# Kernel optimization log

Measured on AMD Instinct MI355X. Metric: run time of the kernel, lower is better.

## Reference

```python
import jax, jax.numpy as jnp
import numpy as np

N = 50000
E = 800000
H, C = 8, 16          # heads, per-head channels (H*C = 128)
G = 64                # number of graphs
EPS = 1e-5


def setup_inputs() -> dict:
    key = jax.random.key(0)
    ks = jax.random.split(key, 8)
    x = jax.random.normal(ks[0], (N, 128), dtype=jnp.float32)
    edge_index = jax.random.randint(ks[1], (2, E), 0, N, dtype=jnp.int64)
    batch = jnp.sort(jax.random.randint(ks[2], (N,), 0, G, dtype=jnp.int64))
    W = jax.random.normal(ks[3], (3, 128, 128), dtype=jnp.float32) * 0.08
    att_src = jax.random.normal(ks[4], (3, H, C), dtype=jnp.float32) * 0.1
    att_dst = jax.random.normal(ks[5], (3, H, C), dtype=jnp.float32) * 0.1
    bias = jnp.zeros((3, 128), dtype=jnp.float32)
    gamma = jnp.ones((3, 128), dtype=jnp.float32)
    beta = jnp.zeros((3, 128), dtype=jnp.float32)
    ro_w = jax.random.normal(ks[6], (128, 2), dtype=jnp.float32) * 0.08
    ro_b = jnp.zeros((2,), dtype=jnp.float32)
    return {"x": x, "edge_index": edge_index, "batch": batch, "W": W,
            "att_src": att_src, "att_dst": att_dst, "bias": bias,
            "gamma": gamma, "beta": beta, "ro_w": ro_w, "ro_b": ro_b}


def _gat_block(prev, h, src, dst, W, a_s, a_d, b, g, be):
    # GATConv (concat=True, add_self_loops already applied to src/dst)
    xp = (h @ W).reshape(N, H, C)                       # [N,H,C]
    al_s = jnp.sum(xp * a_s, axis=-1)                   # [N,H]
    al_d = jnp.sum(xp * a_d, axis=-1)                   # [N,H]
    logits = jax.nn.leaky_relu(al_s[src] + al_d[dst], negative_slope=0.2)  # [Et,H]
    m = jax.ops.segment_max(logits, dst, num_segments=N)        # softmax over dst groups
    ex = jnp.exp(logits - m[dst])
    denom = jax.ops.segment_sum(ex, dst, num_segments=N)
    alpha = ex / denom[dst]                              # [Et,H]
    msg = xp[src] * alpha[:, :, None]                    # [Et,H,C]
    agg = jax.ops.segment_sum(msg, dst, num_segments=N).reshape(N, H * C) + b
    y = prev + agg
    # BatchNorm1d (training mode: batch stats, biased variance)
    mu = y.mean(axis=0)
    var = y.var(axis=0)
    yn = (y - mu) / jnp.sqrt(var + EPS) * g + be
    return jax.nn.elu(yn)


def reference(x, edge_index, batch, W, att_src, att_dst, bias, gamma, beta, ro_w, ro_b):
    loops = jnp.arange(N, dtype=edge_index.dtype)
    src = jnp.concatenate([edge_index[0], loops])        # PyG add_self_loops=True
    dst = jnp.concatenate([edge_index[1], loops])
    h = x
    prev = jnp.zeros((N, 128), dtype=x.dtype)
    for i in range(3):
        out = _gat_block(prev, h, src, dst, W[i], att_src[i], att_dst[i],
                         bias[i], gamma[i], beta[i])
        prev = h[:, :128]
        h = out
    # global mean pool over graphs
    sums = jax.ops.segment_sum(h, batch, num_segments=G)
    cnt = jax.ops.segment_sum(jnp.ones((N,), dtype=h.dtype), batch, num_segments=G)
    pooled = sums / jnp.maximum(cnt, 1.0)[:, None]
    return pooled @ ro_w + ro_b
```

## Files before the change

### kernel.cpp

```cpp
#include <hip/hip_runtime.h>
#include <hip/hip_bf16.h>
#include <math.h>

#define NN 50000
#define EE 800000
#define MM (EE + NN)
#define GG 64
#define SWG 512
#define NSB ((NN + 255) / 256)
#define PSP 16

__device__ __forceinline__ int geti(const void* p, long idx, int is64) {
    return is64 ? (int)((const long long*)p)[idx] : ((const int*)p)[idx];
}

__device__ __forceinline__ float bf2f(unsigned short u) {
    return __uint_as_float(((unsigned)u) << 16);
}

__global__ void k_detect(const int* __restrict__ ei, int* __restrict__ flag) {
    if (blockIdx.x == 0 && threadIdx.x == 0) {
        int ok = 1;
        for (int k = 0; k < 128; ++k) {
            int lo = ei[2 * k], hi = ei[2 * k + 1];
            if (hi != 0 || (unsigned)lo >= (unsigned)NN) { ok = 0; break; }
        }
        flag[0] = ok;
    }
}


__global__ void k_zero(int* p, int n) {
    int i = blockIdx.x * blockDim.x + threadIdx.x;
    if (i < n) p[i] = 0;
}

__global__ void k_count(const void* __restrict__ ei, const int* __restrict__ flag,
                        int* __restrict__ counts) {
    int e = blockIdx.x * blockDim.x + threadIdx.x;
    if (e >= MM) return;
    int is64 = flag[0];
    int d = (e < EE) ? geti(ei, (long)EE + e, is64) : (e - EE);
    if ((unsigned)d < (unsigned)NN) atomicAdd(&counts[d], 1);
}

__global__ __launch_bounds__(256) void k_scan1(const int* __restrict__ counts,
                                               int* __restrict__ rowptr,
                                               int* __restrict__ bsum) {
    __shared__ int buf[256];
    int b = blockIdx.x, tid = threadIdx.x;
    int i = b * 256 + tid;
    int v = (i < NN) ? counts[i] : 0;
    buf[tid] = v;
    __syncthreads();
    for (int off = 1; off < 256; off <<= 1) {
        int t = (tid >= off) ? buf[tid - off] : 0;
        __syncthreads();
        buf[tid] += t;
        __syncthreads();
    }
    if (i < NN) rowptr[i + 1] = buf[tid];
    if (tid == 255) bsum[b] = buf[255];
}

__global__ __launch_bounds__(256) void k_scan2(int* __restrict__ bsum) {
    __shared__ int buf[256];
    int tid = threadIdx.x;
    int v = (tid < NSB) ? bsum[tid] : 0;
    buf[tid] = v;
    __syncthreads();
    for (int off = 1; off < 256; off <<= 1) {
        int t = (tid >= off) ? buf[tid - off] : 0;
        __syncthreads();
        buf[tid] += t;
        __syncthreads();
    }
    if (tid < NSB) bsum[tid] = (tid == 0) ? 0 : buf[tid - 1];
}

__global__ __launch_bounds__(256) void k_scan3(int* __restrict__ rowptr,
                                               const int* __restrict__ bsum) {
    int b = blockIdx.x, tid = threadIdx.x;
    int i = b * 256 + tid;
    if (i < NN) rowptr[i + 1] += bsum[b];
    if (b == 0 && tid == 0) rowptr[0] = 0;
}

__global__ void k_fill(const void* __restrict__ ei, const int* __restrict__ flag,
                       const int* __restrict__ rowptr,
                       int* __restrict__ fill, int* __restrict__ colv) {
    int e = blockIdx.x * blockDim.x + threadIdx.x;
    if (e >= MM) return;
    int is64 = flag[0];
    int s, d;
    if (e < EE) { s = geti(ei, e, is64); d = geti(ei, (long)EE + e, is64); }
    else { s = d = e - EE; }
    if ((unsigned)d >= (unsigned)NN || (unsigned)s >= (unsigned)NN) return;
    int pos = rowptr[d] + atomicAdd(&fill[d], 1);
    if ((unsigned)pos < (unsigned)MM) colv[pos] = s;
}


__global__ __launch_bounds__(256) void k_gemm_att(
    const float* __restrict__ h, const float* __restrict__ W,
    const float* __restrict__ attS, const float* __restrict__ attD,
    unsigned short* __restrict__ xpb, float* __restrict__ als,
    float* __restrict__ ald, int n)
{
    __shared__ float Wt[32][128];
    __shared__ float Ht[128][33];
    int tid = threadIdx.x;
    int head = tid & 7, r0 = tid >> 3;
    int rbase = blockIdx.x * 128;

    float acc[4][16];
#pragma unroll
    for (int a = 0; a < 4; ++a)
#pragma unroll
        for (int b = 0; b < 16; ++b) acc[a][b] = 0.f;

    for (int k0 = 0; k0 < 128; k0 += 32) {
#pragma unroll
        for (int j = 0; j < 4; ++j) {
            int idx = tid * 16 + j * 4;
            int kk = idx >> 7, c = idx & 127;
            *(float4*)&Wt[kk][c] = *(const float4*)&W[(k0 + kk) * 128 + c];
        }
#pragma unroll
        for (int j = 0; j < 4; ++j) {
            int f = tid * 16 + j * 4;
            int r = f >> 5, kk = f & 31;
            int gr = rbase + r;
            float4 v = make_float4(0.f, 0.f, 0.f, 0.f);
            if (gr < n) v = *(const float4*)&h[gr * 128 + k0 + kk];
            Ht[r][kk] = v.x; Ht[r][kk + 1] = v.y; Ht[r][kk + 2] = v.z; Ht[r][kk + 3] = v.w;
        }
        __syncthreads();
#pragma unroll
        for (int kk = 0; kk < 32; ++kk) {
            float wv[16];
#pragma unroll
            for (int j = 0; j < 4; ++j)
                *(float4*)&wv[j * 4] = *(const float4*)&Wt[kk][head * 16 + j * 4];
#pragma unroll
            for (int rr = 0; rr < 4; ++rr) {
                float hv = Ht[r0 + rr * 32][kk];
#pragma unroll
                for (int j = 0; j < 16; ++j) acc[rr][j] = fmaf(hv, wv[j], acc[rr][j]);
            }
        }
        __syncthreads();
    }

    float asv[16], adv[16];
#pragma unroll
    for (int j = 0; j < 16; ++j) { asv[j] = attS[head * 16 + j]; adv[j] = attD[head * 16 + j]; }

#pragma unroll
    for (int rr = 0; rr < 4; ++rr) {
        int r = rbase + r0 + rr * 32;
        if (r < n) {
            float ds = 0.f, dd = 0.f;
#pragma unroll
            for (int j = 0; j < 16; ++j) { ds = fmaf(acc[rr][j], asv[j], ds); dd = fmaf(acc[rr][j], adv[j], dd); }
            als[r * 8 + head] = ds;
            ald[r * 8 + head] = dd;
            unsigned short xb[16];
#pragma unroll
            for (int j = 0; j < 16; ++j) {
                __hip_bfloat16 t = __float2bfloat16(acc[rr][j]);
                xb[j] = *reinterpret_cast<unsigned short*>(&t);
            }
            *(uint4*)&xpb[r * 128 + head * 16]     = *(uint4*)&xb[0];
            *(uint4*)&xpb[r * 128 + head * 16 + 8] = *(uint4*)&xb[8];
        }
    }
}


__global__ __launch_bounds__(256) void k_agg(
    const unsigned short* __restrict__ xpb, const float* __restrict__ als,
    const float* __restrict__ ald,
    const int* __restrict__ rowptr, const int* __restrict__ colv,
    const float* __restrict__ prev, const float* __restrict__ bias,
    float* __restrict__ y, int n)
{
    __shared__ float alds[4][8][8];
    __shared__ int   slds[4][8];
    int wv = threadIdx.x >> 6;
    int wid = (int)((blockIdx.x * blockDim.x + threadIdx.x) >> 6);
    int lane = threadIdx.x & 63;
    if (wid >= n) return;
    int rs = rowptr[wid], re = rowptr[wid + 1];
    int deg = re - rs;

    int hd = lane & 7;
    int ee = lane >> 3;
    float aldn = ald[wid * 8 + hd];

    float sm = 0.f;
    for (int b = ee; b < deg; b += 8) {
        int s = colv[rs + b];
        float v = als[s * 8 + hd] + aldn;
        v = v > 0.f ? v : 0.2f * v;
        sm += expf(v);
    }
    sm += __shfl_xor(sm, 8);
    sm += __shfl_xor(sm, 16);
    sm += __shfl_xor(sm, 32);

    float inv = 1.f / sm;
    int q = lane >> 3;
    int c0 = lane * 2;

    float a0 = 0.f, a1 = 0.f;
    int full = deg & ~7;

    for (int b0 = 0; b0 < full; b0 += 8) {
        int se = colv[rs + b0 + ee];
        float v = als[se * 8 + hd] + aldn;
        v = v > 0.f ? v : 0.2f * v;
        float al = expf(v) * inv;
        alds[wv][ee][hd] = al;
        if (hd == 0) slds[wv][ee] = se;
#pragma unroll
        for (int j = 0; j < 8; ++j) {
            int s = slds[wv][j];
            float a = alds[wv][j][q];
            ushort2 xv = *(const ushort2*)(xpb + (size_t)s * 128 + c0);
            a0 = fmaf(a, bf2f(xv.x), a0);
            a1 = fmaf(a, bf2f(xv.y), a1);
        }
    }

    if (full < deg) {
        int nb = deg - full;
        float al = 0.f;
        int se = 0;
        if (ee < nb) {
            se = colv[rs + full + ee];
            float v = als[se * 8 + hd] + aldn;
            v = v > 0.f ? v : 0.2f * v;
            al = expf(v) * inv;
        }
        alds[wv][ee][hd] = al;
        if (hd == 0) slds[wv][ee] = se;
        for (int j = 0; j < nb; ++j) {
            int s = slds[wv][j];
            float a = alds[wv][j][q];
            ushort2 xv = *(const ushort2*)(xpb + (size_t)s * 128 + c0);
            a0 = fmaf(a, bf2f(xv.x), a0);
            a1 = fmaf(a, bf2f(xv.y), a1);
        }
    }

    float p0 = prev ? prev[wid * 128 + c0] : 0.f;
    float p1 = prev ? prev[wid * 128 + c0 + 1] : 0.f;
    y[wid * 128 + c0] = p0 + a0 + bias[c0];
    y[wid * 128 + c0 + 1] = p1 + a1 + bias[c0 + 1];
}


__global__ __launch_bounds__(256) void k_stats(const float* __restrict__ y,
                                               double* __restrict__ partial, int n) {
    int col = threadIdx.x & 127;
    int rg = threadIdx.x >> 7;
    double s = 0.0, s2 = 0.0;
    for (int r = blockIdx.x * 2 + rg; r < n; r += SWG * 2) {
        float v = y[r * 128 + col];
        s += v; s2 += (double)v * (double)v;
    }
    __shared__ double ls[256], ls2[256];
    ls[threadIdx.x] = s; ls2[threadIdx.x] = s2;
    __syncthreads();
    if (rg == 0) {
        s += ls[threadIdx.x + 128];
        s2 += ls2[threadIdx.x + 128];
        partial[col * SWG + blockIdx.x] = s;
        partial[128 * SWG + col * SWG + blockIdx.x] = s2;
    }
}

__global__ void k_stats_fin(const double* __restrict__ partial, float* __restrict__ stats, int n) {
    int col = threadIdx.x;
    double s = 0.0, s2 = 0.0;
    for (int w = 0; w < SWG; ++w) {
        s += partial[col * SWG + w];
        s2 += partial[128 * SWG + col * SWG + w];
    }
    double mu = s / n;
    double var = s2 / n - mu * mu;
    stats[col] = (float)mu;
    stats[128 + col] = (float)(1.0 / sqrt(var + 1e-5));
}

__global__ __launch_bounds__(256) void k_elem(const float* __restrict__ y,
                                              const float* __restrict__ stats,
                                              const float* __restrict__ gamma,
                                              const float* __restrict__ beta,
                                              float* __restrict__ out, int total)
{
    int i = blockIdx.x * blockDim.x + threadIdx.x;
    if (i >= total) return;
    int col = i & 127;
    float v = (y[i] - stats[col]) * stats[128 + col] * gamma[col] + beta[col];
    out[i] = v > 0.f ? v : expm1f(v);
}


__global__ __launch_bounds__(256) void k_pool_part(
    const float* __restrict__ h, const void* __restrict__ batch,
    const int* __restrict__ flag, float* __restrict__ ppart, int n)
{
    int g = blockIdx.x / PSP;
    int sp = blockIdx.x % PSP;
    int is64 = flag[0];
    int lo = 0, hi = n;
    while (lo < hi) { int mid = (lo + hi) >> 1; if (geti(batch, mid, is64) < g) lo = mid + 1; else hi = mid; }
    int start = lo;
    hi = n;
    while (lo < hi) { int mid = (lo + hi) >> 1; if (geti(batch, mid, is64) < g + 1) lo = mid + 1; else hi = mid; }
    int end = lo;
    int cnt = end - start;
    int slice = (cnt + PSP - 1) / PSP;
    int s0 = start + sp * slice;
    int s1 = s0 + slice; if (s1 > end) s1 = end;

    int col = threadIdx.x & 127;
    int half = threadIdx.x >> 7;
    float s = 0.f;
    for (int r = s0 + half; r < s1; r += 2) s += h[r * 128 + col];
    __shared__ float ls[256];
    ls[threadIdx.x] = s;
    __syncthreads();
    if (half == 0) ppart[(g * PSP + sp) * 128 + col] = s + ls[col + 128];
}

__global__ __launch_bounds__(128) void k_pool_fin(
    const float* __restrict__ ppart, const void* __restrict__ batch,
    const int* __restrict__ flag, const float* __restrict__ row,
    const float* __restrict__ rob, float* __restrict__ out, int n)
{
    int g = blockIdx.x;
    int is64 = flag[0];
    int lo = 0, hi = n;
    while (lo < hi) { int mid = (lo + hi) >> 1; if (geti(batch, mid, is64) < g) lo = mid + 1; else hi = mid; }
    int start = lo;
    hi = n;
    while (lo < hi) { int mid = (lo + hi) >> 1; if (geti(batch, mid, is64) < g + 1) lo = mid + 1; else hi = mid; }
    int cnt = lo - start;

    int col = threadIdx.x;
    float s = 0.f;
#pragma unroll
    for (int sp = 0; sp < PSP; ++sp) s += ppart[(g * PSP + sp) * 128 + col];
    __shared__ float ls[128];
    ls[col] = s * (1.f / fmaxf((float)cnt, 1.f));
    __syncthreads();
    if (col < 2) {
        float acc = 0.f;
        for (int c = 0; c < 128; ++c) acc = fmaf(ls[c], row[c * 2 + col], acc);
        out[g * 2 + col] = acc + rob[col];
    }
}


extern "C" void kernel_launch(void* const* d_in, const int* in_sizes, int n_in,
                              void* d_out, int out_size, void* d_ws, size_t ws_size,
                              hipStream_t stream) {
    const float* x     = (const float*)d_in[0];
    const void*  ei    = d_in[1];
    const void*  batch = d_in[2];
    const float* W     = (const float*)d_in[3];
    const float* attS  = (const float*)d_in[4];
    const float* attD  = (const float*)d_in[5];
    const float* bias  = (const float*)d_in[6];
    const float* gamma = (const float*)d_in[7];
    const float* beta  = (const float*)d_in[8];
    const float* row   = (const float*)d_in[9];
    const float* rob   = (const float*)d_in[10];
    float* out = (float*)d_out;

    char* wsb = (char*)d_ws;
    size_t off = 0;
    auto alloc = [&](size_t bytes) {
        void* p = wsb + off;
        off += (bytes + 255) & ~(size_t)255;
        return p;
    };
    int*    flag    = (int*)alloc(256);
    int*    rowptr  = (int*)alloc((size_t)(NN + 1) * 4);
    int*    cnts    = (int*)alloc((size_t)NN * 4 * 2);
    int*    bsum    = (int*)alloc((size_t)256 * 4);
    int*    colv    = (int*)alloc((size_t)MM * 4);
    double* partial = (double*)alloc((size_t)128 * SWG * 2 * 8);
    float*  stats   = (float*)alloc(256 * 4);
    float*  ppart   = (float*)alloc((size_t)GG * PSP * 128 * 4);
    float*  ALS     = (float*)alloc((size_t)NN * 8 * 4);
    float*  ALD     = (float*)alloc((size_t)NN * 8 * 4);
    unsigned short* XPB = (unsigned short*)alloc((size_t)NN * 128 * 2);
    float* Y   = (float*)alloc((size_t)NN * 128 * 4);
    float* HB1 = (float*)alloc((size_t)NN * 128 * 4);
    float* HB2 = (float*)alloc((size_t)NN * 128 * 4);
    float* H3  = (float*)alloc((size_t)NN * 128 * 4);
    (void)ws_size; (void)in_sizes; (void)n_in; (void)out_size;

    int* fill = cnts + NN;
    const int GE = (NN * 128 + 255) / 256;

    hipLaunchKernelGGL(k_detect, dim3(1), dim3(64), 0, stream, (const int*)ei, flag);
    hipLaunchKernelGGL(k_zero, dim3((2 * NN + 255) / 256), dim3(256), 0, stream, cnts, 2 * NN);
    hipLaunchKernelGGL(k_count, dim3((MM + 255) / 256), dim3(256), 0, stream, ei, flag, cnts);
    hipLaunchKernelGGL(k_scan1, dim3(NSB), dim3(256), 0, stream, cnts, rowptr, bsum);
    hipLaunchKernelGGL(k_scan2, dim3(1), dim3(256), 0, stream, bsum);
    hipLaunchKernelGGL(k_scan3, dim3(NSB), dim3(256), 0, stream, rowptr, bsum);
    hipLaunchKernelGGL(k_fill, dim3((MM + 255) / 256), dim3(256), 0, stream, ei, flag, rowptr, fill, colv);

    const float* hs[4] = { x, HB1, HB2, H3 };
    for (int b = 0; b < 3; ++b) {
        const float* h = hs[b];
        const float* prev = (b == 0) ? nullptr : hs[b - 1];
        float* hn = (float*)hs[b + 1];

        hipLaunchKernelGGL(k_gemm_att, dim3((NN + 127) / 128), dim3(256), 0, stream,
                           h, W + b * 16384, attS + b * 128, attD + b * 128, XPB, ALS, ALD, NN);
        hipLaunchKernelGGL(k_agg, dim3((NN + 3) / 4), dim3(256), 0, stream,
                           XPB, ALS, ALD, rowptr, colv, prev, bias + b * 128, Y, NN);
        hipLaunchKernelGGL(k_stats, dim3(SWG), dim3(256), 0, stream, Y, partial, NN);
        hipLaunchKernelGGL(k_stats_fin, dim3(1), dim3(128), 0, stream, partial, stats, NN);
        hipLaunchKernelGGL(k_elem, dim3(GE), dim3(256), 0, stream,
                           Y, stats, gamma + b * 128, beta + b * 128, hn, NN * 128);
    }

    hipLaunchKernelGGL(k_pool_part, dim3(GG * PSP), dim3(256), 0, stream,
                       hs[3], batch, flag, ppart, NN);
    hipLaunchKernelGGL(k_pool_fin, dim3(GG), dim3(128), 0, stream,
                       ppart, batch, flag, row, rob, out, NN);
}
```

Measured before the change: 581.6 us.

## Fuse BatchNorm+ELU into consumer kernels and drop the elementwise pass

The separate BatchNorm-apply+ELU kernel is removed. The stats kernel now emits a folded per-column scale and shift, and the normalize+ELU is recomputed on the fly wherever the activation is consumed: the GEMM tile load, the residual 'prev' read in aggregation, and the final pooling. This saves a full N×128 read and write per layer plus three launches, at the cost of redundant expm1 evaluations and keeping three raw Y buffers alive.

```diff
diff --git a/kernel.cpp b/kernel.cpp
--- a/kernel.cpp
+++ b/kernel.cpp
@@ -16,6 +16,10 @@
 
 __device__ __forceinline__ float bf2f(unsigned short u) {
     return __uint_as_float(((unsigned)u) << 16);
+}
+
+__device__ __forceinline__ float eluf(float z) {
+    return z > 0.f ? z : expm1f(z);
 }
 
 __global__ void k_detect(const int* __restrict__ ei, int* __restrict__ flag) {
@@ -102,7 +106,8 @@
 
 
 __global__ __launch_bounds__(256) void k_gemm_att(
-    const float* __restrict__ h, const float* __restrict__ W,
+    const float* __restrict__ hsrc, const float* __restrict__ Ysrc,
+    const float* __restrict__ st, const float* __restrict__ W,
     const float* __restrict__ attS, const float* __restrict__ attD,
     unsigned short* __restrict__ xpb, float* __restrict__ als,
     float* __restrict__ ald, int n)
@@ -112,6 +117,7 @@
     int tid = threadIdx.x;
     int head = tid & 7, r0 = tid >> 3;
     int rbase = blockIdx.x * 128;
+    bool useY = (Ysrc != nullptr);
 
     float acc[4][16];
 #pragma unroll
@@ -132,7 +138,19 @@
             int r = f >> 5, kk = f & 31;
             int gr = rbase + r;
             float4 v = make_float4(0.f, 0.f, 0.f, 0.f);
-            if (gr < n) v = *(const float4*)&h[gr * 128 + k0 + kk];
+            if (gr < n) {
+                if (useY) {
+                    float4 yv = *(const float4*)&Ysrc[gr * 128 + k0 + kk];
+                    float4 scv = *(const float4*)&st[k0 + kk];
+                    float4 shv = *(const float4*)&st[128 + k0 + kk];
+                    v.x = eluf(fmaf(yv.x, scv.x, shv.x));
+                    v.y = eluf(fmaf(yv.y, scv.y, shv.y));
+                    v.z = eluf(fmaf(yv.z, scv.z, shv.z));
+                    v.w = eluf(fmaf(yv.w, scv.w, shv.w));
+                } else {
+                    v = *(const float4*)&hsrc[gr * 128 + k0 + kk];
+                }
+            }
             Ht[r][kk] = v.x; Ht[r][kk + 1] = v.y; Ht[r][kk + 2] = v.z; Ht[r][kk + 3] = v.w;
         }
         __syncthreads();
@@ -182,7 +200,8 @@
     const unsigned short* __restrict__ xpb, const float* __restrict__ als,
     const float* __restrict__ ald,
     const int* __restrict__ rowptr, const int* __restrict__ colv,
-    const float* __restrict__ prev, const float* __restrict__ bias,
+    const float* __restrict__ prevRaw, const float* __restrict__ prevY,
+    const float* __restrict__ pst, const float* __restrict__ bias,
     float* __restrict__ y, int n)
 {
     __shared__ float alds[4][8][8];
@@ -254,8 +273,15 @@
         }
     }
 
-    float p0 = prev ? prev[wid * 128 + c0] : 0.f;
-    float p1 = prev ? prev[wid * 128 + c0 + 1] : 0.f;
+    float p0 = 0.f, p1 = 0.f;
+    if (prevY) {
+        float2 yv = *(const float2*)(prevY + (size_t)wid * 128 + c0);
+        p0 = eluf(fmaf(yv.x, pst[c0], pst[128 + c0]));
+        p1 = eluf(fmaf(yv.y, pst[c0 + 1], pst[129 + c0]));
+    } else if (prevRaw) {
+        p0 = prevRaw[(size_t)wid * 128 + c0];
+        p1 = prevRaw[(size_t)wid * 128 + c0 + 1];
+    }
     y[wid * 128 + c0] = p0 + a0 + bias[c0];
     y[wid * 128 + c0 + 1] = p1 + a1 + bias[c0 + 1];
 }
@@ -281,7 +307,10 @@
     }
 }
 
-__global__ void k_stats_fin(const double* __restrict__ partial, float* __restrict__ stats, int n) {
+__global__ void k_stats_fin(const double* __restrict__ partial,
+                            const float* __restrict__ gamma,
+                            const float* __restrict__ beta,
+                            float* __restrict__ st, int n) {
     int col = threadIdx.x;
     double s = 0.0, s2 = 0.0;
     for (int w = 0; w < SWG; ++w) {
@@ -290,27 +319,17 @@
     }
     double mu = s / n;
     double var = s2 / n - mu * mu;
-    stats[col] = (float)mu;
-    stats[128 + col] = (float)(1.0 / sqrt(var + 1e-5));
-}
-
-__global__ __launch_bounds__(256) void k_elem(const float* __restrict__ y,
-                                              const float* __restrict__ stats,
-                                              const float* __restrict__ gamma,
-                                              const float* __restrict__ beta,
-                                              float* __restrict__ out, int total)
-{
-    int i = blockIdx.x * blockDim.x + threadIdx.x;
-    if (i >= total) return;
-    int col = i & 127;
-    float v = (y[i] - stats[col]) * stats[128 + col] * gamma[col] + beta[col];
-    out[i] = v > 0.f ? v : expm1f(v);
+    double rsig = 1.0 / sqrt(var + 1e-5);
+    double sc = (double)gamma[col] * rsig;
+    st[col] = (float)sc;
+    st[128 + col] = (float)((double)beta[col] - mu * sc);
 }
 
 
 __global__ __launch_bounds__(256) void k_pool_part(
-    const float* __restrict__ h, const void* __restrict__ batch,
-    const int* __restrict__ flag, float* __restrict__ ppart, int n)
+    const float* __restrict__ Y, const float* __restrict__ st,
+    const void* __restrict__ batch, const int* __restrict__ flag,
+    float* __restrict__ ppart, int n)
 {
     int g = blockIdx.x / PSP;
     int sp = blockIdx.x % PSP;
@@ -328,8 +347,10 @@
 
     int col = threadIdx.x & 127;
     int half = threadIdx.x >> 7;
+    float sc = st[col], sh = st[128 + col];
     float s = 0.f;
-    for (int r = s0 + half; r < s1; r += 2) s += h[r * 128 + col];
+    for (int r = s0 + half; r < s1; r += 2)
+        s += eluf(fmaf(Y[(size_t)r * 128 + col], sc, sh));
     __shared__ float ls[256];
     ls[threadIdx.x] = s;
     __syncthreads();
@@ -394,19 +415,21 @@
     int*    bsum    = (int*)alloc((size_t)256 * 4);
     int*    colv    = (int*)alloc((size_t)MM * 4);
     double* partial = (double*)alloc((size_t)128 * SWG * 2 * 8);
-    float*  stats   = (float*)alloc(256 * 4);
+    float*  st1     = (float*)alloc(256 * 4);
+    float*  st2     = (float*)alloc(256 * 4);
+    float*  st3     = (float*)alloc(256 * 4);
     float*  ppart   = (float*)alloc((size_t)GG * PSP * 128 * 4);
     float*  ALS     = (float*)alloc((size_t)NN * 8 * 4);
     float*  ALD     = (float*)alloc((size_t)NN * 8 * 4);
     unsigned short* XPB = (unsigned short*)alloc((size_t)NN * 128 * 2);
-    float* Y   = (float*)alloc((size_t)NN * 128 * 4);
-    float* HB1 = (float*)alloc((size_t)NN * 128 * 4);
-    float* HB2 = (float*)alloc((size_t)NN * 128 * 4);
-    float* H3  = (float*)alloc((size_t)NN * 128 * 4);
+    float* Y1 = (float*)alloc((size_t)NN * 128 * 4);
+    float* Y2 = (float*)alloc((size_t)NN * 128 * 4);
+    float* Y3 = (float*)alloc((size_t)NN * 128 * 4);
     (void)ws_size; (void)in_sizes; (void)n_in; (void)out_size;
 
     int* fill = cnts + NN;
-    const int GE = (NN * 128 + 255) / 256;
+    const int GB = (NN + 127) / 128;
+    const int GA = (NN + 3) / 4;
 
     hipLaunchKernelGGL(k_detect, dim3(1), dim3(64), 0, stream, (const int*)ei, flag);
     hipLaunchKernelGGL(k_zero, dim3((2 * NN + 255) / 256), dim3(256), 0, stream, cnts, 2 * NN);
@@ -416,24 +439,38 @@
     hipLaunchKernelGGL(k_scan3, dim3(NSB), dim3(256), 0, stream, rowptr, bsum);
     hipLaunchKernelGGL(k_fill, dim3((MM + 255) / 256), dim3(256), 0, stream, ei, flag, rowptr, fill, colv);
 
-    const float* hs[4] = { x, HB1, HB2, H3 };
-    for (int b = 0; b < 3; ++b) {
-        const float* h = hs[b];
-        const float* prev = (b == 0) ? nullptr : hs[b - 1];
-        float* hn = (float*)hs[b + 1];
-
-        hipLaunchKernelGGL(k_gemm_att, dim3((NN + 127) / 128), dim3(256), 0, stream,
-                           h, W + b * 16384, attS + b * 128, attD + b * 128, XPB, ALS, ALD, NN);
-        hipLaunchKernelGGL(k_agg, dim3((NN + 3) / 4), dim3(256), 0, stream,
-                           XPB, ALS, ALD, rowptr, colv, prev, bias + b * 128, Y, NN);
-        hipLaunchKernelGGL(k_stats, dim3(SWG), dim3(256), 0, stream, Y, partial, NN);
-        hipLaunchKernelGGL(k_stats_fin, dim3(1), dim3(128), 0, stream, partial, stats, NN);
-        hipLaunchKernelGGL(k_elem, dim3(GE), dim3(256), 0, stream,
-                           Y, stats, gamma + b * 128, beta + b * 128, hn, NN * 128);
-    }
+    hipLaunchKernelGGL(k_gemm_att, dim3(GB), dim3(256), 0, stream,
+                       x, (const float*)nullptr, (const float*)nullptr,
+                       W, attS, attD, XPB, ALS, ALD, NN);
+    hipLaunchKernelGGL(k_agg, dim3(GA), dim3(256), 0, stream,
+                       XPB, ALS, ALD, rowptr, colv,
+                       (const float*)nullptr, (const float*)nullptr, (const float*)nullptr,
+                       bias, Y1, NN);
+    hipLaunchKernelGGL(k_stats, dim3(SWG), dim3(256), 0, stream, Y1, partial, NN);
+    hipLaunchKernelGGL(k_stats_fin, dim3(1), dim3(128), 0, stream, partial, gamma, beta, st1, NN);
+
+    hipLaunchKernelGGL(k_gemm_att, dim3(GB), dim3(256), 0, stream,
+                       (const float*)nullptr, Y1, st1,
+                       W + 16384, attS + 128, attD + 128, XPB, ALS, ALD, NN);
+    hipLaunchKernelGGL(k_agg, dim3(GA), dim3(256), 0, stream,
+                       XPB, ALS, ALD, rowptr, colv,
+                       x, (const float*)nullptr, (const float*)nullptr,
+                       bias + 128, Y2, NN);
+    hipLaunchKernelGGL(k_stats, dim3(SWG), dim3(256), 0, stream, Y2, partial, NN);
+    hipLaunchKernelGGL(k_stats_fin, dim3(1), dim3(128), 0, stream, partial, gamma + 128, beta + 128, st2, NN);
+
+    hipLaunchKernelGGL(k_gemm_att, dim3(GB), dim3(256), 0, stream,
+                       (const float*)nullptr, Y2, st2,
+                       W + 32768, attS + 256, attD + 256, XPB, ALS, ALD, NN);
+    hipLaunchKernelGGL(k_agg, dim3(GA), dim3(256), 0, stream,
+                       XPB, ALS, ALD, rowptr, colv,
+                       (const float*)nullptr, Y1, st1,
+                       bias + 256, Y3, NN);
+    hipLaunchKernelGGL(k_stats, dim3(SWG), dim3(256), 0, stream, Y3, partial, NN);
+    hipLaunchKernelGGL(k_stats_fin, dim3(1), dim3(128), 0, stream, partial, gamma + 256, beta + 256, st3, NN);
 
     hipLaunchKernelGGL(k_pool_part, dim3(GG * PSP), dim3(256), 0, stream,
-                       hs[3], batch, flag, ppart, NN);
+                       Y3, st3, batch, flag, ppart, NN);
     hipLaunchKernelGGL(k_pool_fin, dim3(GG), dim3(128), 0, stream,
                        ppart, batch, flag, row, rob, out, NN);
 }
```

New measurement: 551.0 us. 5.2% less time.
